# Kernel tuning notes

Hardware: AMD Instinct MI355X
Metric: run time of the kernel (lower is better)

Reference implementation:

```python
import jax, jax.numpy as jnp
import numpy as np

N_GRAPHS = 32
NODES = 4096          # nodes per graph
D_IN = 128
HID = 16
OUT_DIM = 39
N = N_GRAPHS * NODES  # 131072 total nodes
E = N * 32            # avg degree 32 -> 4194304 edges


def setup_inputs() -> dict:
    key = jax.random.key(0)
    ks = jax.random.split(key, 7)
    x = jax.random.normal(ks[0], (N, D_IN), dtype=jnp.float32)
    # edges constrained within each graph (PyG Batch semantics)
    src_local = jax.random.randint(ks[1], (E,), 0, NODES)
    dst_local = jax.random.randint(ks[2], (E,), 0, NODES)
    graph_of_edge = jnp.arange(E, dtype=jnp.int64) % N_GRAPHS
    offset = graph_of_edge * NODES
    edge_index = jnp.stack([src_local.astype(jnp.int64) + offset,
                            dst_local.astype(jnp.int64) + offset], axis=0)
    W_l = jax.random.normal(ks[3], (HID, D_IN), dtype=jnp.float32) * 0.05
    b_l = jnp.zeros((HID,), dtype=jnp.float32)
    W_r = jax.random.normal(ks[4], (HID, D_IN), dtype=jnp.float32) * 0.05
    W_out = jax.random.normal(ks[5], (OUT_DIM, NODES * HID), dtype=jnp.float32) * 0.01
    b_out = jnp.zeros((OUT_DIM,), dtype=jnp.float32)
    return {"x": x, "edge_index": edge_index, "W_l": W_l, "b_l": b_l,
            "W_r": W_r, "W_out": W_out, "b_out": b_out}


def reference(x, edge_index, W_l, b_l, W_r, W_out, b_out):
    src, dst = edge_index[0], edge_index[1]
    # SAGEConv (mean aggr): lin_l(mean_{j in N(i)} x_j) + lin_r(x_i)
    # Linear commutes with mean: transform first (D_IN -> HID) to shrink gather traffic.
    xl = x @ W_l.T                                      # [N, HID]
    agg = jax.ops.segment_sum(xl[src], dst, num_segments=N)   # [N, HID]
    cnt = jax.ops.segment_sum(jnp.ones((E,), x.dtype), dst, num_segments=N)
    mean = agg / jnp.maximum(cnt, 1.0)[:, None]         # zero-degree nodes -> 0
    h = jax.nn.relu(mean + b_l + x @ W_r.T)             # [N, HID]
    # per-graph flatten + shared Linear (the Python loop in torch == batched matmul)
    g = h.reshape(N_GRAPHS, NODES * HID)                # [G, NODES*HID]
    out = g @ W_out.T + b_out                           # [G, OUT_DIM]
    return out[:, :, None]                              # [G, OUT_DIM, 1] (unsqueeze(1) per-graph, stacked)
```

## Files before the change

kernel.cpp:

```cpp
#include <hip/hip_runtime.h>

#define NG 32
#define NODES 4096
#define NTOT (NG * NODES)
#define DIN 128
#define HID 16
#define ODIM 39
#define NEDGE (NTOT * 32)
#define EPG (NEDGE / NG)
#define CH  32
#define CHE 4096

typedef unsigned int uint;
typedef unsigned short ushort;

#define NB   8192
#define BCAP 768

#define K4B  1024
#define PODS 40

#define WS_XL     0
#define WS_XR     2097152
#define WS_AGG    4194304
#define WS_CNT    6291456
#define WS_GCOUNT 6422528
#define PEDGE_BYTE_OFF  ((size_t)(6422528 + 8192) * 4)
#define HIST2_BYTE_OFF  (PEDGE_BYTE_OFF + (size_t)NB * BCAP * 2)
#define SEED2_BYTE_OFF  (HIST2_BYTE_OFF + (size_t)NG * CH * 256 * 4)
#define PEDGE0_BYTE_OFF (SEED2_BYTE_OFF + (size_t)NG * CH * 256 * 4)
#define WS_NEED_FAST    (PEDGE0_BYTE_OFF + (size_t)NEDGE * 4)

__global__ __launch_bounds__(256) void k1_lin(const float* __restrict__ x,
                                              const float* __restrict__ Wl,
                                              const float* __restrict__ Wr,
                                              float* __restrict__ xl,
                                              float* __restrict__ xr) {
    __shared__ float xs[64 * 132];
    __shared__ float wls[16 * 132];
    __shared__ float wrs[16 * 132];
    const int t = threadIdx.x;

    #pragma unroll
    for (int i = 0; i < 2; ++i) {
        int f = i * 256 + t;
        int o = f >> 5, k4 = f & 31;
        float4 a = reinterpret_cast<const float4*>(Wl)[f];
        float4 b = reinterpret_cast<const float4*>(Wr)[f];
        *reinterpret_cast<float4*>(&wls[o * 132 + 4 * k4]) = a;
        *reinterpret_cast<float4*>(&wrs[o * 132 + 4 * k4]) = b;
    }

    const long base = (long)blockIdx.x * 64;
    const float4* xg = reinterpret_cast<const float4*>(x) + base * 32;
    #pragma unroll
    for (int i = 0; i < 8; ++i) {
        int f = i * 256 + t;
        int n = f >> 5, k4 = f & 31;
        *reinterpret_cast<float4*>(&xs[n * 132 + 4 * k4]) = xg[f];
    }
    __syncthreads();

    const int o = t & 15, ngrp = t >> 4;
    float accl[4] = {0.f, 0.f, 0.f, 0.f};
    float accr[4] = {0.f, 0.f, 0.f, 0.f};
    for (int k4 = 0; k4 < 32; ++k4) {
        float4 w0 = *reinterpret_cast<const float4*>(&wls[o * 132 + 4 * k4]);
        float4 w1 = *reinterpret_cast<const float4*>(&wrs[o * 132 + 4 * k4]);
        #pragma unroll
        for (int j = 0; j < 4; ++j) {
            float4 xv = *reinterpret_cast<const float4*>(&xs[(ngrp + 16 * j) * 132 + 4 * k4]);
            accl[j] += xv.x * w0.x + xv.y * w0.y + xv.z * w0.z + xv.w * w0.w;
            accr[j] += xv.x * w1.x + xv.y * w1.y + xv.z * w1.z + xv.w * w1.w;
        }
    }
    #pragma unroll
    for (int j = 0; j < 4; ++j) {
        long n = base + ngrp + 16 * j;
        xl[n * HID + o] = accl[j];
        xr[n * HID + o] = accr[j];
    }
}

__global__ __launch_bounds__(1024) void kT_pack(const int* __restrict__ ei,
                                                uint* __restrict__ pedge0) {
    __shared__ uint st[32 * 129];
    const int b = blockIdx.x;
    const int t = threadIdx.x;
    const int e0 = b * 4096;
    #pragma unroll
    for (int j = 0; j < 4; ++j) {
        int e = e0 + j * 1024 + t;
        uint s = (uint)ei[e] & 4095u;
        uint d = (uint)ei[NEDGE + e] & 4095u;
        int g = e & 31;
        int i = (e >> 5) & 127;
        st[g * 129 + i] = s | (d << 16);
    }
    __syncthreads();
    #pragma unroll
    for (int j = 0; j < 4; ++j) {
        int o = j * 1024 + t;
        int g = o >> 7, i = o & 127;
        pedge0[(size_t)g * EPG + b * 128 + i] = st[g * 129 + i];
    }
}

__global__ __launch_bounds__(256) void kH2(const uint* __restrict__ pedge0,
                                           uint* __restrict__ hist2) {
    __shared__ uint lh[256];
    const int bid = blockIdx.x;
    const int g = bid >> 5, c = bid & 31;
    const int t = threadIdx.x;
    lh[t] = 0u;
    __syncthreads();
    const uint4* pe = reinterpret_cast<const uint4*>(pedge0 + (size_t)g * EPG + c * CHE);
    #pragma unroll
    for (int j = 0; j < 4; ++j) {
        uint4 p = pe[j * 256 + t];
        atomicAdd(&lh[(p.x >> 20) & 255], 1u);
        atomicAdd(&lh[(p.y >> 20) & 255], 1u);
        atomicAdd(&lh[(p.z >> 20) & 255], 1u);
        atomicAdd(&lh[(p.w >> 20) & 255], 1u);
    }
    __syncthreads();
    hist2[(size_t)bid * 256 + t] = lh[t];
}

__global__ __launch_bounds__(256) void kScan2(const uint* __restrict__ hist2,
                                              uint* __restrict__ seed2,
                                              uint* __restrict__ gcount) {
    const int g = blockIdx.x;
    const int t = threadIdx.x;
    uint run = 0u;
    for (int c = 0; c < CH; ++c) {
        size_t idx = (size_t)(g * CH + c) * 256 + t;
        uint v = hist2[idx];
        seed2[idx] = run;
        run += v;
    }
    gcount[g * 256 + t] = run;
}

__global__ __launch_bounds__(256) void kB3(const uint* __restrict__ pedge0,
                                           const uint* __restrict__ hist2,
                                           const uint* __restrict__ seed2,
                                           ushort* __restrict__ pedge) {
    __shared__ ushort sorted[CHE];
    __shared__ uint tgt[CHE];
    __shared__ uint lstart[256];
    __shared__ uint gseed[256];
    __shared__ uint cur[256];
    __shared__ uint wsum[4];
    const int bid = blockIdx.x;
    const int g = bid >> 5, c = bid & 31;
    const int t = threadIdx.x;
    const int lane = t & 63, w = t >> 6;

    const uint v = hist2[(size_t)bid * 256 + t];
    gseed[t] = seed2[(size_t)bid * 256 + t];

    const uint4* pe = reinterpret_cast<const uint4*>(pedge0 + (size_t)g * EPG + c * CHE);
    uint4 loc[4];
    #pragma unroll
    for (int j = 0; j < 4; ++j) loc[j] = pe[j * 256 + t];

    {
        uint inc = v;
        #pragma unroll
        for (int off = 1; off < 64; off <<= 1) {
            uint u = __shfl_up(inc, off, 64);
            if (lane >= off) inc += u;
        }
        if (lane == 63) wsum[w] = inc;
        __syncthreads();
        uint base = 0u;
        #pragma unroll
        for (int ww = 0; ww < 4; ++ww)
            if (ww < w) base += wsum[ww];
        uint ls = base + inc - v;
        lstart[t] = ls;
        cur[t] = ls;
    }
    __syncthreads();

    #pragma unroll
    for (int j = 0; j < 4; ++j) {
        uint p;
        #pragma unroll
        for (int q = 0; q < 4; ++q) {
            p = (q == 0) ? loc[j].x : (q == 1) ? loc[j].y : (q == 2) ? loc[j].z : loc[j].w;
            uint s = (p >> 20) & 255u;
            uint idx = atomicAdd(&cur[s], 1u);
            sorted[idx] = (ushort)((p & 4095u) | (((p >> 16) & 15u) << 12));
            tgt[idx] = (s << 10) | (gseed[s] + (idx - lstart[s]));
        }
    }
    __syncthreads();

    #pragma unroll
    for (int it = 0; it < CHE / 256; ++it) {
        int i = it * 256 + t;
        uint tg = tgt[i];
        uint s = tg >> 10, pos = tg & 1023u;
        if (pos < BCAP)
            pedge[(size_t)(g * 256 + s) * BCAP + pos] = sorted[i];
    }
}

__global__ __launch_bounds__(256) void kS_reg(const uint* __restrict__ gcount,
                                              const ushort* __restrict__ pedge,
                                              const float* __restrict__ xl,
                                              float* __restrict__ agg,
                                              float* __restrict__ cnt) {
    __shared__ ushort eb[BCAP];
    __shared__ ushort sorted[BCAP];
    __shared__ uint c16[16];
    __shared__ uint off16[16];
    __shared__ uint cur16[16];
    __shared__ float4 part[16 * 4 * 4];
    const int b = blockIdx.x;
    const int g = b >> 8, seg = b & 255;
    const int t = threadIdx.x;

    if (t < 16) c16[t] = 0u;
    int n = (int)gcount[b];
    if (n > BCAP) n = BCAP;
    const size_t bo = (size_t)b * BCAP;
    __syncthreads();

    for (int i = t; i < n; i += 256) {
        ushort p = pedge[bo + i];
        eb[i] = p;
        atomicAdd(&c16[p >> 12], 1u);
    }
    __syncthreads();

    if (t == 0) {
        uint run = 0u;
        #pragma unroll
        for (int d = 0; d < 16; ++d) {
            off16[d] = run;
            cur16[d] = run;
            run += c16[d];
        }
    }
    __syncthreads();

    for (int i = t; i < n; i += 256) {
        ushort p = eb[i];
        uint pos = atomicAdd(&cur16[p >> 12], 1u);
        sorted[pos] = (ushort)(p & 4095u);
    }
    __syncthreads();

    const int dlo = t >> 4;
    const int qi  = (t >> 2) & 3;
    const int ch4 = t & 3;
    const uint start = off16[dlo];
    const uint len = c16[dlo];
    const float4* xrow4 = reinterpret_cast<const float4*>(xl + (((size_t)g << 12) * HID)) + ch4;
    float4 acc = {0.f, 0.f, 0.f, 0.f};
    for (uint i = qi; i < len; i += 4) {
        int sl = sorted[start + i];
        float4 v = xrow4[sl * 4];
        acc.x += v.x; acc.y += v.y; acc.z += v.z; acc.w += v.w;
    }
    part[t] = acc;
    __syncthreads();

    if (t < 64) {
        int d = t >> 2, c4 = t & 3;
        float4 p0 = part[d * 16 + 0 * 4 + c4];
        float4 p1 = part[d * 16 + 1 * 4 + c4];
        float4 p2 = part[d * 16 + 2 * 4 + c4];
        float4 p3 = part[d * 16 + 3 * 4 + c4];
        float4 s;
        s.x = (p0.x + p1.x) + (p2.x + p3.x);
        s.y = (p0.y + p1.y) + (p2.y + p3.y);
        s.z = (p0.z + p1.z) + (p2.z + p3.z);
        s.w = (p0.w + p1.w) + (p2.w + p3.w);
        float* ga = agg + (((size_t)g << 12) + (seg << 4) + d) * HID + c4 * 4;
        *reinterpret_cast<float4*>(ga) = s;
    }
    if (t < 16) cnt[((size_t)g << 12) + (seg << 4) + t] = (float)c16[t];
}

__global__ __launch_bounds__(256, 4) void k4b_out(const float* __restrict__ agg,
                                                  const float* __restrict__ cnt,
                                                  const float* __restrict__ xr,
                                                  const float* __restrict__ bl,
                                                  const float* __restrict__ Wout,
                                                  float* __restrict__ partial) {
    __shared__ float hs[32 * 64];
    __shared__ float wt[39 * 68];
    const int t = threadIdx.x;
    const int kb = blockIdx.x;
    const int kbase = kb * 64;

    #pragma unroll
    for (int r = 0; r < 8; ++r) {
        int idx = r * 256 + t;
        int g = idx >> 6, kk = idx & 63;
        long flat = (long)g * (NODES * HID) + kbase + kk;
        float a = agg[flat];
        float xv = xr[flat];
        float cn = cnt[(g << 12) + ((kbase + kk) >> 4)];
        float h = a / fmaxf(cn, 1.0f) + bl[kk & 15] + xv;
        hs[g * 64 + kk] = fmaxf(h, 0.0f);
    }
    for (int idx = t; idx < ODIM * 64; idx += 256) {
        int od = idx >> 6, kk = idx & 63;
        wt[od * 68 + kk] = Wout[(long)od * (NODES * HID) + kbase + kk];
    }
    __syncthreads();

    const int tod = t & 31, tg = t >> 5;
    const int od0 = tod;
    const bool has1 = (tod + 32) < ODIM;
    const int od1 = has1 ? tod + 32 : tod;
    float acc0[4] = {0.f, 0.f, 0.f, 0.f};
    float acc1[4] = {0.f, 0.f, 0.f, 0.f};
    #pragma unroll 4
    for (int k4 = 0; k4 < 16; ++k4) {
        float4 w0 = *reinterpret_cast<const float4*>(&wt[od0 * 68 + 4 * k4]);
        float4 w1 = *reinterpret_cast<const float4*>(&wt[od1 * 68 + 4 * k4]);
        #pragma unroll
        for (int j = 0; j < 4; ++j) {
            float4 h4 = *reinterpret_cast<const float4*>(&hs[(tg * 4 + j) * 64 + 4 * k4]);
            acc0[j] += h4.x * w0.x + h4.y * w0.y + h4.z * w0.z + h4.w * w0.w;
            acc1[j] += h4.x * w1.x + h4.y * w1.y + h4.z * w1.z + h4.w * w1.w;
        }
    }
    float* pb = partial + (size_t)kb * (NG * PODS);
    #pragma unroll
    for (int j = 0; j < 4; ++j) {
        int g = tg * 4 + j;
        pb[g * PODS + od0] = acc0[j];
        if (has1) pb[g * PODS + od1] = acc1[j];
    }
}

__global__ __launch_bounds__(256) void kR2_reduce(const float* __restrict__ partial,
                                                  const float* __restrict__ bout,
                                                  float* __restrict__ out) {
    const int b = blockIdx.x;
    const int g = b / PODS, od = b - g * PODS;
    if (od >= ODIM) return;
    const int t = threadIdx.x;
    const float* p = partial + g * PODS + od;
    float acc = 0.f;
    #pragma unroll
    for (int i = 0; i < K4B / 256; ++i)
        acc += p[(size_t)(i * 256 + t) * (NG * PODS)];
    #pragma unroll
    for (int off = 32; off > 0; off >>= 1)
        acc += __shfl_down(acc, off, 64);
    __shared__ float w4[4];
    if ((t & 63) == 0) w4[t >> 6] = acc;
    __syncthreads();
    if (t == 0)
        out[g * ODIM + od] = w4[0] + w4[1] + w4[2] + w4[3] + bout[od];
}

__global__ __launch_bounds__(256) void k2_edges(const int* __restrict__ ei,
                                                const float* __restrict__ xl,
                                                float* __restrict__ agg,
                                                float* __restrict__ cnt) {
    const long tid = (long)blockIdx.x * 256 + threadIdx.x;
    const int e = (int)(tid >> 4);
    const int c = (int)(tid & 15);
    const int s = ei[e];
    const int d = ei[NEDGE + e];
    const float v = xl[(long)s * HID + c];
    atomicAdd(&agg[(long)d * HID + c], v);
    if (c == 0) atomicAdd(&cnt[d], 1.0f);
}

__global__ __launch_bounds__(256) void k3_init_out(const float* __restrict__ bout,
                                                   float* __restrict__ out) {
    int i = blockIdx.x * 256 + threadIdx.x;
    if (i < NG * ODIM) out[i] = bout[i % ODIM];
}

__global__ __launch_bounds__(256) void k4_out(const float* __restrict__ agg,
                                              const float* __restrict__ cnt,
                                              const float* __restrict__ xr,
                                              const float* __restrict__ bl,
                                              const float* __restrict__ Wout,
                                              float* __restrict__ out) {
    __shared__ float hs[32 * 128];
    __shared__ float wt[39 * 132];
    const int t = threadIdx.x;
    const int kbase = blockIdx.x * 128;

    #pragma unroll
    for (int r = 0; r < 16; ++r) {
        int idx = r * 256 + t;
        int g = idx >> 7, kk = idx & 127;
        long flat = (long)g * (NODES * HID) + kbase + kk;
        float a = agg[flat];
        float xv = xr[flat];
        float cn = cnt[(g << 12) + ((kbase + kk) >> 4)];
        float h = a / fmaxf(cn, 1.0f) + bl[kk & 15] + xv;
        hs[g * 128 + kk] = fmaxf(h, 0.0f);
    }
    for (int idx = t; idx < ODIM * 128; idx += 256) {
        int od = idx >> 7, kk = idx & 127;
        wt[od * 132 + kk] = Wout[(long)od * (NODES * HID) + kbase + kk];
    }
    __syncthreads();

    const int tod = t & 31, tg = t >> 5;
    const int od0 = tod;
    const bool has1 = (tod + 32) < ODIM;
    const int od1 = has1 ? tod + 32 : tod;
    float acc0[4] = {0.f, 0.f, 0.f, 0.f};
    float acc1[4] = {0.f, 0.f, 0.f, 0.f};
    for (int k4 = 0; k4 < 32; ++k4) {
        float4 w0 = *reinterpret_cast<const float4*>(&wt[od0 * 132 + 4 * k4]);
        float4 w1 = *reinterpret_cast<const float4*>(&wt[od1 * 132 + 4 * k4]);
        #pragma unroll
        for (int j = 0; j < 4; ++j) {
            float4 h4 = *reinterpret_cast<const float4*>(&hs[(tg * 4 + j) * 128 + 4 * k4]);
            acc0[j] += h4.x * w0.x + h4.y * w0.y + h4.z * w0.z + h4.w * w0.w;
            acc1[j] += h4.x * w1.x + h4.y * w1.y + h4.z * w1.z + h4.w * w1.w;
        }
    }
    #pragma unroll
    for (int j = 0; j < 4; ++j) {
        int g = tg * 4 + j;
        atomicAdd(&out[g * ODIM + od0], acc0[j]);
        if (has1) atomicAdd(&out[g * ODIM + od1], acc1[j]);
    }
}

extern "C" void kernel_launch(void* const* d_in, const int* in_sizes, int n_in,
                              void* d_out, int out_size, void* d_ws, size_t ws_size,
                              hipStream_t stream) {
    const float* x    = (const float*)d_in[0];
    const int*   ei   = (const int*)d_in[1];
    const float* Wl   = (const float*)d_in[2];
    const float* bl   = (const float*)d_in[3];
    const float* Wr   = (const float*)d_in[4];
    const float* Wout = (const float*)d_in[5];
    const float* bout = (const float*)d_in[6];
    float* out = (float*)d_out;
    float* ws  = (float*)d_ws;

    float* xl  = ws + WS_XL;
    float* xr  = ws + WS_XR;
    float* agg = ws + WS_AGG;
    float* cnt = ws + WS_CNT;

    if (ws_size >= WS_NEED_FAST) {
        uint*   gcount  = (uint*)(ws + WS_GCOUNT);
        ushort* pedge   = (ushort*)((char*)d_ws + PEDGE_BYTE_OFF);
        uint*   hist2   = (uint*)((char*)d_ws + HIST2_BYTE_OFF);
        uint*   seed2   = (uint*)((char*)d_ws + SEED2_BYTE_OFF);
        uint*   pedge0  = (uint*)((char*)d_ws + PEDGE0_BYTE_OFF);
        float*  partial = (float*)((char*)d_ws + PEDGE_BYTE_OFF);

        k1_lin<<<NTOT / 64, 256, 0, stream>>>(x, Wl, Wr, xl, xr);
        kT_pack<<<NEDGE / 4096, 1024, 0, stream>>>(ei, pedge0);
        kH2<<<NG * CH, 256, 0, stream>>>(pedge0, hist2);
        kScan2<<<NG, 256, 0, stream>>>(hist2, seed2, gcount);
        kB3<<<NG * CH, 256, 0, stream>>>(pedge0, hist2, seed2, pedge);
        kS_reg<<<NB, 256, 0, stream>>>(gcount, pedge, xl, agg, cnt);
        k4b_out<<<K4B, 256, 0, stream>>>(agg, cnt, xr, bl, Wout, partial);
        kR2_reduce<<<NG * PODS, 256, 0, stream>>>(partial, bout, out);
    } else {
        hipMemsetAsync(agg, 0, (size_t)(NTOT * HID + NTOT) * sizeof(float), stream);
        k1_lin<<<NTOT / 64, 256, 0, stream>>>(x, Wl, Wr, xl, xr);
        k2_edges<<<(long)NEDGE * 16 / 256, 256, 0, stream>>>(ei, xl, agg, cnt);
        k3_init_out<<<(NG * ODIM + 255) / 256, 256, 0, stream>>>(bout, out);
        k4_out<<<(NODES * HID) / 128, 256, 0, stream>>>(agg, cnt, xr, bl, Wout, out);
    }
}
```

Before: 116.3 us.

## Compute per-node degree in histogram pass; skip counting pass in segment kernel

The histogram kernel now bins edges by full 12-bit destination (4096 bins), derives the 256-bucket histogram from it, and accumulates per-node degree counts globally with atomics. The segment kernel then reads these counts directly, so it no longer needs a staging copy and a counting atomic pass over its edges. It also reads packed 16-bit edges two at a time and uses two accumulators in the gather loop to expose more memory-level parallelism. The trade-off is a larger shared histogram, global atomics into a new count buffer, and an extra memset.

```diff
diff --git a/kernel.cpp b/kernel.cpp
--- a/kernel.cpp
+++ b/kernel.cpp
@@ -29,7 +29,8 @@
 #define HIST2_BYTE_OFF  (PEDGE_BYTE_OFF + (size_t)NB * BCAP * 2)
 #define SEED2_BYTE_OFF  (HIST2_BYTE_OFF + (size_t)NG * CH * 256 * 4)
 #define PEDGE0_BYTE_OFF (SEED2_BYTE_OFF + (size_t)NG * CH * 256 * 4)
-#define WS_NEED_FAST    (PEDGE0_BYTE_OFF + (size_t)NEDGE * 4)
+#define CNTU_BYTE_OFF   (PEDGE0_BYTE_OFF + (size_t)NEDGE * 4)
+#define WS_NEED_FAST    (CNTU_BYTE_OFF + (size_t)NTOT * 4)
 
 __global__ __launch_bounds__(256) void k1_lin(const float* __restrict__ x,
                                               const float* __restrict__ Wl,
@@ -107,24 +108,32 @@
 }
 
 __global__ __launch_bounds__(256) void kH2(const uint* __restrict__ pedge0,
-                                           uint* __restrict__ hist2) {
-    __shared__ uint lh[256];
+                                           uint* __restrict__ hist2,
+                                           uint* __restrict__ cntU) {
+    __shared__ uint lh[4096];
     const int bid = blockIdx.x;
     const int g = bid >> 5, c = bid & 31;
     const int t = threadIdx.x;
-    lh[t] = 0u;
+    for (int i = t; i < 4096; i += 256) lh[i] = 0u;
     __syncthreads();
     const uint4* pe = reinterpret_cast<const uint4*>(pedge0 + (size_t)g * EPG + c * CHE);
     #pragma unroll
     for (int j = 0; j < 4; ++j) {
         uint4 p = pe[j * 256 + t];
-        atomicAdd(&lh[(p.x >> 20) & 255], 1u);
-        atomicAdd(&lh[(p.y >> 20) & 255], 1u);
-        atomicAdd(&lh[(p.z >> 20) & 255], 1u);
-        atomicAdd(&lh[(p.w >> 20) & 255], 1u);
-    }
-    __syncthreads();
-    hist2[(size_t)bid * 256 + t] = lh[t];
+        atomicAdd(&lh[(p.x >> 16) & 4095], 1u);
+        atomicAdd(&lh[(p.y >> 16) & 4095], 1u);
+        atomicAdd(&lh[(p.z >> 16) & 4095], 1u);
+        atomicAdd(&lh[(p.w >> 16) & 4095], 1u);
+    }
+    __syncthreads();
+    uint s = 0u;
+    #pragma unroll
+    for (int j = 0; j < 16; ++j) s += lh[t * 16 + j];
+    hist2[(size_t)bid * 256 + t] = s;
+    for (int i = t; i < 4096; i += 256) {
+        uint v = lh[i];
+        if (v) atomicAdd(&cntU[(g << 12) + i], v);
+    }
 }
 
 __global__ __launch_bounds__(256) void kScan2(const uint* __restrict__ hist2,
@@ -208,34 +217,23 @@
     }
 }
 
-__global__ __launch_bounds__(256) void kS_reg(const uint* __restrict__ gcount,
+__global__ __launch_bounds__(256) void kS_reg(const uint* __restrict__ cntU,
                                               const ushort* __restrict__ pedge,
                                               const float* __restrict__ xl,
                                               float* __restrict__ agg,
                                               float* __restrict__ cnt) {
-    __shared__ ushort eb[BCAP];
     __shared__ ushort sorted[BCAP];
     __shared__ uint c16[16];
     __shared__ uint off16[16];
     __shared__ uint cur16[16];
+    __shared__ uint ntot;
     __shared__ float4 part[16 * 4 * 4];
     const int b = blockIdx.x;
     const int g = b >> 8, seg = b & 255;
     const int t = threadIdx.x;
 
-    if (t < 16) c16[t] = 0u;
-    int n = (int)gcount[b];
-    if (n > BCAP) n = BCAP;
-    const size_t bo = (size_t)b * BCAP;
-    __syncthreads();
-
-    for (int i = t; i < n; i += 256) {
-        ushort p = pedge[bo + i];
-        eb[i] = p;
-        atomicAdd(&c16[p >> 12], 1u);
-    }
-    __syncthreads();
-
+    if (t < 16) c16[t] = cntU[b * 16 + t];
+    __syncthreads();
     if (t == 0) {
         uint run = 0u;
         #pragma unroll
@@ -244,28 +242,55 @@
             cur16[d] = run;
             run += c16[d];
         }
-    }
-    __syncthreads();
-
-    for (int i = t; i < n; i += 256) {
-        ushort p = eb[i];
-        uint pos = atomicAdd(&cur16[p >> 12], 1u);
-        sorted[pos] = (ushort)(p & 4095u);
+        ntot = (run > BCAP) ? BCAP : run;
+    }
+    __syncthreads();
+
+    const int n = (int)ntot;
+    const uint* pe32 = reinterpret_cast<const uint*>(pedge + (size_t)b * BCAP);
+    for (int i2 = t; i2 * 2 < n; i2 += 256) {
+        uint pp = pe32[i2];
+        {
+            uint p0 = pp & 0xFFFFu;
+            uint pos = atomicAdd(&cur16[p0 >> 12], 1u);
+            if (pos < BCAP) sorted[pos] = (ushort)(p0 & 4095u);
+        }
+        if (i2 * 2 + 1 < n) {
+            uint p1 = pp >> 16;
+            uint pos = atomicAdd(&cur16[p1 >> 12], 1u);
+            if (pos < BCAP) sorted[pos] = (ushort)(p1 & 4095u);
+        }
     }
     __syncthreads();
 
     const int dlo = t >> 4;
     const int qi  = (t >> 2) & 3;
     const int ch4 = t & 3;
-    const uint start = off16[dlo];
-    const uint len = c16[dlo];
+    uint start = off16[dlo];
+    uint len = 0u;
+    if (start < BCAP) {
+        uint end = cur16[dlo];
+        if (end > BCAP) end = BCAP;
+        len = (end > start) ? (end - start) : 0u;
+    }
     const float4* xrow4 = reinterpret_cast<const float4*>(xl + (((size_t)g << 12) * HID)) + ch4;
-    float4 acc = {0.f, 0.f, 0.f, 0.f};
-    for (uint i = qi; i < len; i += 4) {
+    float4 acc  = {0.f, 0.f, 0.f, 0.f};
+    float4 acc2 = {0.f, 0.f, 0.f, 0.f};
+    uint i = qi;
+    for (; i + 4 < len; i += 8) {
+        int sl0 = sorted[start + i];
+        int sl1 = sorted[start + i + 4];
+        float4 v0 = xrow4[sl0 * 4];
+        float4 v1 = xrow4[sl1 * 4];
+        acc.x  += v0.x; acc.y  += v0.y; acc.z  += v0.z; acc.w  += v0.w;
+        acc2.x += v1.x; acc2.y += v1.y; acc2.z += v1.z; acc2.w += v1.w;
+    }
+    if (i < len) {
         int sl = sorted[start + i];
         float4 v = xrow4[sl * 4];
         acc.x += v.x; acc.y += v.y; acc.z += v.z; acc.w += v.w;
     }
+    acc.x += acc2.x; acc.y += acc2.y; acc.z += acc2.z; acc.w += acc2.w;
     part[t] = acc;
     __syncthreads();
 
@@ -459,14 +484,16 @@
         uint*   hist2   = (uint*)((char*)d_ws + HIST2_BYTE_OFF);
         uint*   seed2   = (uint*)((char*)d_ws + SEED2_BYTE_OFF);
         uint*   pedge0  = (uint*)((char*)d_ws + PEDGE0_BYTE_OFF);
+        uint*   cntU    = (uint*)((char*)d_ws + CNTU_BYTE_OFF);
         float*  partial = (float*)((char*)d_ws + PEDGE_BYTE_OFF);
 
+        hipMemsetAsync(cntU, 0, (size_t)NTOT * sizeof(uint), stream);
         k1_lin<<<NTOT / 64, 256, 0, stream>>>(x, Wl, Wr, xl, xr);
         kT_pack<<<NEDGE / 4096, 1024, 0, stream>>>(ei, pedge0);
-        kH2<<<NG * CH, 256, 0, stream>>>(pedge0, hist2);
+        kH2<<<NG * CH, 256, 0, stream>>>(pedge0, hist2, cntU);
         kScan2<<<NG, 256, 0, stream>>>(hist2, seed2, gcount);
         kB3<<<NG * CH, 256, 0, stream>>>(pedge0, hist2, seed2, pedge);
-        kS_reg<<<NB, 256, 0, stream>>>(gcount, pedge, xl, agg, cnt);
+        kS_reg<<<NB, 256, 0, stream>>>(cntU, pedge, xl, agg, cnt);
         k4b_out<<<K4B, 256, 0, stream>>>(agg, cnt, xr, bl, Wout, partial);
         kR2_reduce<<<NG * PODS, 256, 0, stream>>>(partial, bout, out);
     } else {
```

Result: slower. 133.0 us (+14.3%).
